# Performance work log

Measured on AMD Instinct MI355X. Metric: run time of the kernel, lower is better.

Reference implementation:

```python
import jax, jax.numpy as jnp
import numpy as np

B, C, L, D = 8, 32, 2048, 128
R, H = 8, 4  # num_routers, num_heads


def setup_inputs() -> dict:
    key = jax.random.key(0)
    ks = jax.random.split(key, 20)
    p = lambda k, shape: jax.random.normal(k, shape, dtype=jnp.float32) * 0.02
    inp = {
        "Z": jax.random.normal(ks[0], (B, C, L, D), dtype=jnp.float32),
        "router": p(ks[1], (R, D)),
        # router_sender projections (d_model -> d_model, torch Linear stored as x@W+b)
        "Wq1": p(ks[2], (D, D)), "bq1": jnp.zeros((D,), jnp.float32),
        "Wk1": p(ks[3], (D, D)), "bk1": jnp.zeros((D,), jnp.float32),
        "Wv1": p(ks[4], (D, D)), "bv1": jnp.zeros((D,), jnp.float32),
        "Wo1": p(ks[5], (D, D)), "bo1": jnp.zeros((D,), jnp.float32),
        # router_receiver projections
        "Wq2": p(ks[6], (D, D)), "bq2": jnp.zeros((D,), jnp.float32),
        "Wk2": p(ks[7], (D, D)), "bk2": jnp.zeros((D,), jnp.float32),
        "Wv2": p(ks[8], (D, D)), "bv2": jnp.zeros((D,), jnp.float32),
        "Wo2": p(ks[9], (D, D)), "bo2": jnp.zeros((D,), jnp.float32),
        # LayerNorm
        "gamma": jnp.ones((D,), jnp.float32),
        "beta": jnp.zeros((D,), jnp.float32),
    }
    return inp


def _cross_attn(q_in, k_in, v_in, Wq, bq, Wk, bk, Wv, bv, Wo, bo):
    # Informer FullAttention + AttentionLayer (dropout=0)
    Bn, Lq, Dm = q_in.shape
    Lk = k_in.shape[1]
    dh = Dm // H
    q = (q_in @ Wq + bq).reshape(Bn, Lq, H, dh)
    k = (k_in @ Wk + bk).reshape(Bn, Lk, H, dh)
    v = (v_in @ Wv + bv).reshape(Bn, Lk, H, dh)
    scale = 1.0 / np.sqrt(dh)
    scores = jnp.einsum("blhe,bshe->bhls", q, k) * scale
    A = jax.nn.softmax(scores, axis=-1)
    out = jnp.einsum("bhls,bshd->blhd", A, v).reshape(Bn, Lq, Dm)
    return out @ Wo + bo


def _layernorm(x, gamma, beta, eps=1e-5):
    mu = jnp.mean(x, axis=-1, keepdims=True)
    var = jnp.mean(jnp.square(x - mu), axis=-1, keepdims=True)
    return (x - mu) * jax.lax.rsqrt(var + eps) * gamma + beta


def reference(Z, router, Wq1, bq1, Wk1, bk1, Wv1, bv1, Wo1, bo1,
              Wq2, bq2, Wk2, bk2, Wv2, bv2, Wo2, bo2, gamma, beta):
    Bz, Cz, Lz, Dz = Z.shape
    x = Z.reshape(Bz * Cz, Lz, Dz)
    batch_router = jnp.broadcast_to(router[None], (Bz * Cz, R, Dz))
    # stage 1: routers attend to the sequence (R x L)
    router_buffer = _cross_attn(batch_router, x, x,
                                Wq1, bq1, Wk1, bk1, Wv1, bv1, Wo1, bo1)
    # stage 2: sequence attends to routers (L x R)
    router_receive = _cross_attn(x, router_buffer, router_buffer,
                                 Wq2, bq2, Wk2, bk2, Wv2, bv2, Wo2, bo2)
    out = _layernorm(x + router_receive, gamma, beta)
    return out.reshape(Bz, Cz, Lz, Dz)
```

## Files before the change

### kernel.cpp

```cpp
#include <hip/hip_runtime.h>

typedef float f4_t __attribute__((ext_vector_type(4)));
typedef __bf16 bf8_t __attribute__((ext_vector_type(8)));
typedef __bf16 bf4_t __attribute__((ext_vector_type(4)));

#define MFMA16(a,b,c) __builtin_amdgcn_mfma_f32_16x16x32_bf16((a),(b),(c),0,0,0)

static constexpr float kScale = 0.17677669529663687f;

__device__ __forceinline__ void bar_lds() {
  asm volatile("s_waitcnt lgkmcnt(0)" ::: "memory");
  __builtin_amdgcn_s_barrier();
}

__global__ __launch_bounds__(256) void k0_fold(
    const float* __restrict__ router, const float* __restrict__ Wq1,
    const float* __restrict__ bq1, const float* __restrict__ Wk1,
    const float* __restrict__ bk1, __bf16* __restrict__ q1t,
    float* __restrict__ c1)
{
  __shared__ float q1[8][132];
  const int t = threadIdx.x, b = blockIdx.x;
  {
    const int dp = t & 127, rh = t >> 7;
    float acc[4] = {0.f, 0.f, 0.f, 0.f};
#pragma unroll 4
    for (int e = 0; e < 128; ++e) {
      float wq = Wq1[e*128 + dp];
#pragma unroll
      for (int i = 0; i < 4; ++i)
        acc[i] += router[(rh*4 + i)*128 + e] * wq;
    }
#pragma unroll
    for (int i = 0; i < 4; ++i)
      q1[rh*4 + i][dp] = acc[i] + bq1[dp];
  }
  __syncthreads();
  {
    const int j = t & 31, h = j >> 3, r = j & 7;
    const int e = b*8 + (t >> 5);
    f4_t qv[8];
#pragma unroll
    for (int d4 = 0; d4 < 8; ++d4)
      qv[d4] = *(const f4_t*)&q1[r][h*32 + d4*4];
    float acc = 0.f;
#pragma unroll
    for (int d4 = 0; d4 < 8; ++d4) {
      f4_t wv = *(const f4_t*)(Wk1 + e*128 + h*32 + d4*4);
#pragma unroll
      for (int i = 0; i < 4; ++i) acc += qv[d4][i] * wv[i];
    }
    q1t[j*128 + e] = (__bf16)(acc * kScale);
  }
  if (b == 0 && t < 32) {
    int h = t >> 3, r = t & 7;
    float acc = 0.f;
    for (int d = 0; d < 32; ++d) acc += q1[r][h*32 + d] * bk1[h*32 + d];
    c1[t] = acc * kScale;
  }
}

__global__ __launch_bounds__(512) void k1_stage1(
    const float* __restrict__ Z, const __bf16* __restrict__ q1t_g,
    const float* __restrict__ c1_g, float* __restrict__ xap,
    float* __restrict__ lp, __bf16* __restrict__ xws)
{
  __shared__ __bf16 xb[64][136];
  __shared__ __bf16 xT[128][72];
  __shared__ __bf16 PT[32][72];
  __shared__ float lds_l[32];

  const int tid = threadIdx.x;
  const int bid = blockIdx.x;
  const float* xbase = Z + (size_t)bid * (256 * 128);
  __bf16* xwb = xws + (size_t)bid * (256 * 128);

  if (tid < 32) lds_l[tid] = 0.f;

  const int lane = tid & 63;
  const int w = tid >> 6;
  const int lc = lane & 15;
  const int lg = lane >> 4;
  const int ms = w >> 2;
  const int ns = w & 3;
  float c1v[4];
#pragma unroll
  for (int r2 = 0; r2 < 4; ++r2) c1v[r2] = c1_g[ms*16 + lg*4 + r2];
  bf8_t aq[4];
#pragma unroll
  for (int ks = 0; ks < 4; ++ks)
    aq[ks] = *(const bf8_t*)(q1t_g + (ms*16 + lc)*128 + ks*32 + lg*8);

  const f4_t fzero = {0.f, 0.f, 0.f, 0.f};
  f4_t accxa[2] = { fzero, fzero };
  float Lacc[4] = {0.f, 0.f, 0.f, 0.f};

  const int srow = tid >> 4;
  const int sd0  = (tid & 15) << 3;

  f4_t zr[4];
#pragma unroll
  for (int i = 0; i < 2; ++i) {
    const float* p = xbase + (srow + 32*i)*128 + sd0;
    zr[i*2]   = __builtin_nontemporal_load((const f4_t*)p);
    zr[i*2+1] = __builtin_nontemporal_load((const f4_t*)(p + 4));
  }

  bar_lds();

  for (int tile = 0; tile < 4; ++tile) {
#pragma unroll
    for (int i = 0; i < 2; ++i) {
      int pos = srow + 32*i;
      f4_t v0 = zr[i*2], v1 = zr[i*2+1];
      bf8_t b8 = { (__bf16)v0.x, (__bf16)v0.y, (__bf16)v0.z, (__bf16)v0.w,
                   (__bf16)v1.x, (__bf16)v1.y, (__bf16)v1.z, (__bf16)v1.w };
      *(bf8_t*)&xb[pos][sd0] = b8;
      *(bf8_t*)(xwb + (tile*64 + pos)*128 + sd0) = b8;
    }
    bar_lds();

    if (tile < 3) {
      const float* xt = xbase + (tile + 1) * (64 * 128);
#pragma unroll
      for (int i = 0; i < 2; ++i) {
        const float* p = xt + (srow + 32*i)*128 + sd0;
        zr[i*2]   = __builtin_nontemporal_load((const f4_t*)p);
        zr[i*2+1] = __builtin_nontemporal_load((const f4_t*)(p + 4));
      }
    }

#pragma unroll
    for (int s = 0; s < 2; ++s) {
      int u = tid + s*512;
      int dim = u & 127, pb = (u >> 7) << 3;
      bf8_t t8;
#pragma unroll
      for (int p = 0; p < 8; ++p) t8[p] = xb[pb + p][dim];
      *(bf8_t*)&xT[dim][pb] = t8;
    }
    f4_t sacc = fzero;
#pragma unroll
    for (int ks = 0; ks < 4; ++ks) {
      bf8_t b = *(const bf8_t*)&xb[ns*16 + lc][ks*32 + lg*8];
      sacc = MFMA16(aq[ks], b, sacc);
    }
    const int posn = ns*16 + lc;
#pragma unroll
    for (int r2 = 0; r2 < 4; ++r2) {
      float p = __expf(sacc[r2] + c1v[r2]);
      Lacc[r2] += p;
      PT[ms*16 + lg*4 + r2][posn] = (__bf16)p;
    }
    bar_lds();

#pragma unroll
    for (int nt = 0; nt < 2; ++nt) {
      const int dimt = (ns << 1) + nt;
#pragma unroll
      for (int ks = 0; ks < 2; ++ks) {
        bf8_t a = *(const bf8_t*)&xT[dimt*16 + lc][ks*32 + lg*8];
        bf8_t b = *(const bf8_t*)&PT[ms*16 + lc][ks*32 + lg*8];
        accxa[nt] = MFMA16(a, b, accxa[nt]);
      }
    }
  }

#pragma unroll
  for (int r2 = 0; r2 < 4; ++r2) {
    float v = Lacc[r2];
    v += __shfl_xor(v, 1);
    v += __shfl_xor(v, 2);
    v += __shfl_xor(v, 4);
    v += __shfl_xor(v, 8);
    if (lc == 0) atomicAdd(&lds_l[ms*16 + lg*4 + r2], v);
  }
  bar_lds();

  float* xo = xap + (size_t)bid * 4096;
  const int jrow = ms*16 + lc;
#pragma unroll
  for (int nt = 0; nt < 2; ++nt) {
    const int dim0 = ((ns << 1) + nt)*16 + lg*4;
    *(f4_t*)(xo + jrow*128 + dim0) = accxa[nt];
  }
  if (tid < 32) lp[bid*32 + tid] = lds_l[tid];
}

__global__ __launch_bounds__(256) void k1b_mid(
    const float* __restrict__ xap, const float* __restrict__ lp,
    const float* __restrict__ Wv1, const float* __restrict__ bv1,
    const float* __restrict__ Wo1, const float* __restrict__ bo1,
    const float* __restrict__ Wk2, const float* __restrict__ bk2,
    const float* __restrict__ Wv2, const float* __restrict__ bv2,
    const float* __restrict__ Wq2, const float* __restrict__ bq2,
    const float* __restrict__ Wo2,
    __bf16* __restrict__ kt2, float* __restrict__ c2, __bf16* __restrict__ vt2)
{
  __shared__ float xaT[128][33];
  __shared__ float invl[32];
  __shared__ float out1T[128][12];
  __shared__ float rbT[128][12];
  __shared__ float k2s[8][136];
  __shared__ float v2s[8][136];

  const int t = threadIdx.x, b = blockIdx.x;

  for (int idx = t; idx < 4096; idx += 256) {
    int j = idx >> 7, e = idx & 127;
    float s = 0.f;
#pragma unroll
    for (int k = 0; k < 8; ++k)
      s += xap[(size_t)(b*8 + k) * 4096 + idx];
    xaT[e][j] = s;
  }
  if (t < 32) {
    float s = 0.f;
#pragma unroll
    for (int k = 0; k < 8; ++k) s += lp[(b*8 + k)*32 + t];
    invl[t] = 1.f / s;
  }
  bar_lds();

  {
    const int hd = t & 127, rh = t >> 7, h = hd >> 5, j0 = h*8 + rh*4;
    float acc[4] = {0.f, 0.f, 0.f, 0.f};
#pragma unroll 4
    for (int e = 0; e < 128; ++e) {
      float wv = Wv1[e*128 + hd];
#pragma unroll
      for (int i = 0; i < 4; ++i) acc[i] += xaT[e][j0 + i] * wv;
    }
    float bv = bv1[hd];
#pragma unroll
    for (int i = 0; i < 4; ++i)
      out1T[hd][rh*4 + i] = acc[i] * invl[j0 + i] + bv;
  }
  bar_lds();

  {
    const int e2 = t & 127, rh = t >> 7;
    float acc[4] = {0.f, 0.f, 0.f, 0.f};
#pragma unroll 4
    for (int hd = 0; hd < 128; ++hd) {
      float wo = Wo1[hd*128 + e2];
#pragma unroll
      for (int i = 0; i < 4; ++i) acc[i] += out1T[hd][rh*4 + i] * wo;
    }
    float bo = bo1[e2];
#pragma unroll
    for (int i = 0; i < 4; ++i) rbT[e2][rh*4 + i] = acc[i] + bo;
  }
  bar_lds();

  {
    const int hd = t & 127, sel = t >> 7;
    const float* W  = sel ? Wv2 : Wk2;
    const float* bb = sel ? bv2 : bk2;
    float (*dst)[136] = sel ? v2s : k2s;
    float acc[8];
    float bbv = bb[hd];
#pragma unroll
    for (int r = 0; r < 8; ++r) acc[r] = bbv;
#pragma unroll 4
    for (int e = 0; e < 128; ++e) {
      float wv = W[e*128 + hd];
#pragma unroll
      for (int r = 0; r < 8; ++r) acc[r] += rbT[e][r] * wv;
    }
#pragma unroll
    for (int r = 0; r < 8; ++r) dst[r][hd] = acc[r];
  }
  bar_lds();

  {
    const int j = t & 31, h = j >> 3, r = j & 7;
    const int esub = t >> 5;
    f4_t k2v[8], v2v[8];
#pragma unroll
    for (int d4 = 0; d4 < 8; ++d4) {
      k2v[d4] = *(const f4_t*)&k2s[r][h*32 + d4*4];
      v2v[d4] = *(const f4_t*)&v2s[r][h*32 + d4*4];
    }
#pragma unroll
    for (int ei = 0; ei < 16; ++ei) {
      const int e = esub + ei*8;
      float acck = 0.f, accv = 0.f;
#pragma unroll
      for (int d4 = 0; d4 < 8; ++d4) {
        f4_t wq = *(const f4_t*)(Wq2 + e*128 + h*32 + d4*4);
#pragma unroll
        for (int i = 0; i < 4; ++i) {
          acck += wq[i] * k2v[d4][i];
          accv += v2v[d4][i] * Wo2[(h*32 + d4*4 + i)*128 + e];
        }
      }
      kt2[(size_t)b*4096 + j*128 + e] = (__bf16)(acck * kScale);
      vt2[(size_t)b*4096 + e*32 + j] = (__bf16)accv;
    }
  }
  if (t < 32) {
    int h = t >> 3, r = t & 7;
    float acc = 0.f;
#pragma unroll
    for (int d = 0; d < 32; ++d) acc += bq2[h*32 + d] * k2s[r][h*32 + d];
    c2[b*32 + t] = acc * kScale;
  }
}

__global__ __launch_bounds__(512) void k2_stage2(
    const __bf16* __restrict__ xws, const __bf16* __restrict__ kt2,
    const float* __restrict__ c2g, const __bf16* __restrict__ vt2,
    const float* __restrict__ bo2, const float* __restrict__ gamma,
    const float* __restrict__ beta, float* __restrict__ out)
{
  __shared__ __bf16 xb[128][136];
  __shared__ __bf16 P2[128][40];

  const int tid = threadIdx.x;
  const int blk = blockIdx.x;
  const int batch = blk >> 1;

  const __bf16* ktb = kt2 + (size_t)batch * 4096;
  const __bf16* vtb = vt2 + (size_t)batch * 4096;

  const int lane = tid & 63;
  const int w = tid >> 6;
  const int lc = lane & 15;
  const int lg = lane >> 4;

  float c2v[2] = { c2g[batch*32 + lc], c2g[batch*32 + 16 + lc] };
  f4_t bo2v[8], gv[8], bv[8];
#pragma unroll
  for (int nt = 0; nt < 8; ++nt) {
    int dd = nt*16 + lg*4;
    bo2v[nt] = *(const f4_t*)(bo2 + dd);
    gv[nt]   = *(const f4_t*)(gamma + dd);
    bv[nt]   = *(const f4_t*)(beta + dd);
  }
  bf8_t vfrag[8];
#pragma unroll
  for (int nt = 0; nt < 8; ++nt)
    vfrag[nt] = *(const bf8_t*)(vtb + (nt*16 + lc)*32 + lg*8);

  int spos[4], sd[4];
#pragma unroll
  for (int j = 0; j < 4; ++j) {
    int c = lane + j*64;
    spos[j] = w*16 + (c >> 4);
    sd[j]   = (c & 15) << 3;
  }

  const size_t base0 = (size_t)blk * 8 * 16384;
  uint4 zx[4];
#pragma unroll
  for (int j = 0; j < 4; ++j)
    zx[j] = *(const uint4*)(xws + base0 + spos[j]*128 + sd[j]);

  const f4_t fzero = {0.f, 0.f, 0.f, 0.f};

  for (int c = 0; c < 8; ++c) {
    const size_t cb = base0 + (size_t)c * 16384;
#pragma unroll
    for (int j = 0; j < 4; ++j)
      *(uint4*)&xb[spos[j]][sd[j]] = zx[j];
    if (c < 7) {
#pragma unroll
      for (int j = 0; j < 4; ++j)
        zx[j] = *(const uint4*)(xws + cb + 16384 + spos[j]*128 + sd[j]);
    }

    f4_t sacc[2] = { fzero, fzero };
#pragma unroll
    for (int ks = 0; ks < 4; ++ks) {
      bf8_t a = *(const bf8_t*)&xb[w*16 + lc][ks*32 + lg*8];
#pragma unroll
      for (int nt = 0; nt < 2; ++nt) {
        bf8_t b = *(const bf8_t*)(ktb + (nt*16 + lc)*128 + ks*32 + lg*8);
        sacc[nt] = MFMA16(a, b, sacc[nt]);
      }
    }
#pragma unroll
    for (int nt = 0; nt < 2; ++nt) {
#pragma unroll
      for (int r2 = 0; r2 < 4; ++r2) {
        float p = __expf(sacc[nt][r2] + c2v[nt]);
        float sum = p;
        sum += __shfl_xor(sum, 1);
        sum += __shfl_xor(sum, 2);
        sum += __shfl_xor(sum, 4);
        P2[w*16 + lg*4 + r2][nt*16 + lc] = (__bf16)(p * __builtin_amdgcn_rcpf(sum));
      }
    }

    bf8_t pf = *(const bf8_t*)&P2[w*16 + lc][lg*8];
    f4_t racc[8];
#pragma unroll
    for (int nt = 0; nt < 8; ++nt)
      racc[nt] = MFMA16(vfrag[nt], pf, fzero);

    const int pos = w*16 + lc;
    float s1 = 0.f, s2 = 0.f;
#pragma unroll
    for (int nt = 0; nt < 8; ++nt) {
      bf4_t xq = *(const bf4_t*)&xb[pos][nt*16 + lg*4];
#pragma unroll
      for (int r = 0; r < 4; ++r) {
        float tv = racc[nt][r] + bo2v[nt][r] + (float)xq[r];
        racc[nt][r] = tv;
        s1 += tv; s2 += tv*tv;
      }
    }
    s1 += __shfl_xor(s1, 16); s1 += __shfl_xor(s1, 32);
    s2 += __shfl_xor(s2, 16); s2 += __shfl_xor(s2, 32);
    float mean = s1 * (1.f/128.f);
    float var = s2 * (1.f/128.f) - mean*mean;
    float rstd = rsqrtf(var + 1e-5f);

    float* y = out + cb + (size_t)pos*128;
#pragma unroll
    for (int nt = 0; nt < 8; ++nt) {
      f4_t o;
#pragma unroll
      for (int r = 0; r < 4; ++r)
        o[r] = (racc[nt][r] - mean) * rstd * gv[nt][r] + bv[nt][r];
      __builtin_nontemporal_store(o, (f4_t*)(y + nt*16 + lg*4));
    }
  }
}

extern "C" void kernel_launch(void* const* d_in, const int* in_sizes, int n_in,
                              void* d_out, int out_size, void* d_ws, size_t ws_size,
                              hipStream_t stream)
{
  const float* Z     = (const float*)d_in[0];
  const float* router= (const float*)d_in[1];
  const float* Wq1   = (const float*)d_in[2];
  const float* bq1   = (const float*)d_in[3];
  const float* Wk1   = (const float*)d_in[4];
  const float* bk1   = (const float*)d_in[5];
  const float* Wv1   = (const float*)d_in[6];
  const float* bv1   = (const float*)d_in[7];
  const float* Wo1   = (const float*)d_in[8];
  const float* bo1   = (const float*)d_in[9];
  const float* Wq2   = (const float*)d_in[10];
  const float* bq2   = (const float*)d_in[11];
  const float* Wk2   = (const float*)d_in[12];
  const float* bk2   = (const float*)d_in[13];
  const float* Wv2   = (const float*)d_in[14];
  const float* bv2   = (const float*)d_in[15];
  const float* Wo2   = (const float*)d_in[16];
  const float* bo2   = (const float*)d_in[17];
  const float* gamma = (const float*)d_in[18];
  const float* beta  = (const float*)d_in[19];
  float* out = (float*)d_out;

  char* base = (char*)d_ws;
  __bf16* q1tb = (__bf16*)(base);
  float*  c1   = (float*)(base + 8192);
  float*  c2   = (float*)(base + 16384);
  float*  lp   = (float*)(base + 65536);
  float*  xap  = (float*)(base + (1u<<20));
  __bf16* kt2b = (__bf16*)(base + (36u<<20));
  __bf16* vt2b = (__bf16*)(base + (38u<<20));
  __bf16* xws  = (__bf16*)(base + (40u<<20));
  (void)in_sizes; (void)n_in; (void)out_size; (void)ws_size;

  k0_fold<<<dim3(16), dim3(256), 0, stream>>>(router, Wq1, bq1, Wk1, bk1, q1tb, c1);
  k1_stage1<<<dim3(2048), dim3(512), 0, stream>>>(Z, q1tb, c1, xap, lp, xws);
  k1b_mid<<<dim3(256), dim3(256), 0, stream>>>(xap, lp, Wv1, bv1, Wo1, bo1,
                                               Wk2, bk2, Wv2, bv2, Wq2, bq2, Wo2,
                                               kt2b, c2, vt2b);
  k2_stage2<<<dim3(512), dim3(512), 0, stream>>>(xws, kt2b, c2, vt2b, bo2, gamma, beta, out);
}
```

Before: 276.0 us.

## Fuse mid-stage router projections into stage-2 kernel, dropping a launch

```diff
diff --git a/kernel.cpp b/kernel.cpp
--- a/kernel.cpp
+++ b/kernel.cpp
@@ -187,95 +187,120 @@
   if (tid < 32) lp[bid*32 + tid] = lds_l[tid];
 }
 
-__global__ __launch_bounds__(256) void k1b_mid(
-    const float* __restrict__ xap, const float* __restrict__ lp,
+__global__ __launch_bounds__(512) void k2_stage2(
+    const __bf16* __restrict__ xws, const float* __restrict__ xap,
+    const float* __restrict__ lp,
     const float* __restrict__ Wv1, const float* __restrict__ bv1,
     const float* __restrict__ Wo1, const float* __restrict__ bo1,
     const float* __restrict__ Wk2, const float* __restrict__ bk2,
     const float* __restrict__ Wv2, const float* __restrict__ bv2,
     const float* __restrict__ Wq2, const float* __restrict__ bq2,
-    const float* __restrict__ Wo2,
-    __bf16* __restrict__ kt2, float* __restrict__ c2, __bf16* __restrict__ vt2)
+    const float* __restrict__ Wo2, const float* __restrict__ bo2,
+    const float* __restrict__ gamma, const float* __restrict__ beta,
+    float* __restrict__ out)
 {
-  __shared__ float xaT[128][33];
-  __shared__ float invl[32];
-  __shared__ float out1T[128][12];
-  __shared__ float rbT[128][12];
-  __shared__ float k2s[8][136];
-  __shared__ float v2s[8][136];
-
-  const int t = threadIdx.x, b = blockIdx.x;
-
-  for (int idx = t; idx < 4096; idx += 256) {
+  __shared__ __align__(16) char smem[64256];
+  __bf16 (*xb)[136]  = (__bf16 (*)[136])(smem);
+  __bf16 (*P2)[40]   = (__bf16 (*)[40])(smem + 34816);
+  __bf16 (*ktL)[136] = (__bf16 (*)[136])(smem + 45056);
+  __bf16 (*vtL)[40]  = (__bf16 (*)[40])(smem + 53760);
+  float* c2L  = (float*)(smem + 64000);
+  float* invl = (float*)(smem + 64128);
+  float (*xaT)[33]   = (float (*)[33])(smem);
+  float (*out1T)[12] = (float (*)[12])(smem + 16896);
+  float (*rbT)[12]   = (float (*)[12])(smem + 23040);
+  float (*k2s)[136]  = (float (*)[136])(smem);
+  float (*v2s)[136]  = (float (*)[136])(smem + 4352);
+
+  const int tid = threadIdx.x;
+  const int blk = blockIdx.x;
+  const int batch = blk >> 1;
+
+  const int lane = tid & 63;
+  const int w = tid >> 6;
+  const int lc = lane & 15;
+  const int lg = lane >> 4;
+
+  int spos[4], sd[4];
+#pragma unroll
+  for (int j = 0; j < 4; ++j) {
+    int c = lane + j*64;
+    spos[j] = w*16 + (c >> 4);
+    sd[j]   = (c & 15) << 3;
+  }
+  const size_t base0 = (size_t)blk * 8 * 16384;
+  uint4 zx[4];
+#pragma unroll
+  for (int j = 0; j < 4; ++j)
+    zx[j] = *(const uint4*)(xws + base0 + spos[j]*128 + sd[j]);
+
+#pragma unroll
+  for (int i = 0; i < 8; ++i) {
+    int idx = tid + i*512;
     int j = idx >> 7, e = idx & 127;
     float s = 0.f;
 #pragma unroll
     for (int k = 0; k < 8; ++k)
-      s += xap[(size_t)(b*8 + k) * 4096 + idx];
+      s += xap[(size_t)(batch*8 + k) * 4096 + idx];
     xaT[e][j] = s;
   }
-  if (t < 32) {
+  if (tid < 32) {
     float s = 0.f;
 #pragma unroll
-    for (int k = 0; k < 8; ++k) s += lp[(b*8 + k)*32 + t];
-    invl[t] = 1.f / s;
-  }
-  bar_lds();
-
-  {
-    const int hd = t & 127, rh = t >> 7, h = hd >> 5, j0 = h*8 + rh*4;
-    float acc[4] = {0.f, 0.f, 0.f, 0.f};
+    for (int k = 0; k < 8; ++k) s += lp[(batch*8 + k)*32 + tid];
+    invl[tid] = 1.f / s;
+  }
+  bar_lds();
+  {
+    const int hd = tid & 127, rh = tid >> 7, h = hd >> 5;
+    const int j0 = h*8 + rh*2;
+    float acc[2] = {0.f, 0.f};
 #pragma unroll 4
     for (int e = 0; e < 128; ++e) {
       float wv = Wv1[e*128 + hd];
-#pragma unroll
-      for (int i = 0; i < 4; ++i) acc[i] += xaT[e][j0 + i] * wv;
+      acc[0] += xaT[e][j0] * wv;
+      acc[1] += xaT[e][j0 + 1] * wv;
     }
     float bv = bv1[hd];
-#pragma unroll
-    for (int i = 0; i < 4; ++i)
-      out1T[hd][rh*4 + i] = acc[i] * invl[j0 + i] + bv;
-  }
-  bar_lds();
-
-  {
-    const int e2 = t & 127, rh = t >> 7;
-    float acc[4] = {0.f, 0.f, 0.f, 0.f};
+    out1T[hd][rh*2]     = acc[0] * invl[j0] + bv;
+    out1T[hd][rh*2 + 1] = acc[1] * invl[j0 + 1] + bv;
+  }
+  bar_lds();
+  {
+    const int e2 = tid & 127, rh = tid >> 7;
+    float acc[2] = {0.f, 0.f};
 #pragma unroll 4
     for (int hd = 0; hd < 128; ++hd) {
       float wo = Wo1[hd*128 + e2];
-#pragma unroll
-      for (int i = 0; i < 4; ++i) acc[i] += out1T[hd][rh*4 + i] * wo;
+      acc[0] += out1T[hd][rh*2] * wo;
+      acc[1] += out1T[hd][rh*2 + 1] * wo;
     }
     float bo = bo1[e2];
-#pragma unroll
-    for (int i = 0; i < 4; ++i) rbT[e2][rh*4 + i] = acc[i] + bo;
-  }
-  bar_lds();
-
-  {
-    const int hd = t & 127, sel = t >> 7;
+    rbT[e2][rh*2]     = acc[0] + bo;
+    rbT[e2][rh*2 + 1] = acc[1] + bo;
+  }
+  bar_lds();
+  {
+    const int hd = tid & 127, q = tid >> 7;
+    const int sel = q >> 1, r0 = (q & 1) * 4;
     const float* W  = sel ? Wv2 : Wk2;
     const float* bb = sel ? bv2 : bk2;
     float (*dst)[136] = sel ? v2s : k2s;
-    float acc[8];
     float bbv = bb[hd];
-#pragma unroll
-    for (int r = 0; r < 8; ++r) acc[r] = bbv;
+    float acc[4] = {bbv, bbv, bbv, bbv};
 #pragma unroll 4
     for (int e = 0; e < 128; ++e) {
       float wv = W[e*128 + hd];
 #pragma unroll
-      for (int r = 0; r < 8; ++r) acc[r] += rbT[e][r] * wv;
-    }
-#pragma unroll
-    for (int r = 0; r < 8; ++r) dst[r][hd] = acc[r];
-  }
-  bar_lds();
-
-  {
-    const int j = t & 31, h = j >> 3, r = j & 7;
-    const int esub = t >> 5;
+      for (int i = 0; i < 4; ++i) acc[i] += rbT[e][r0 + i] * wv;
+    }
+#pragma unroll
+    for (int i = 0; i < 4; ++i) dst[r0 + i][hd] = acc[i];
+  }
+  bar_lds();
+  {
+    const int j = tid & 31, h = j >> 3, r = j & 7;
+    const int esub = tid >> 5;
     f4_t k2v[8], v2v[8];
 #pragma unroll
     for (int d4 = 0; d4 < 8; ++d4) {
@@ -283,8 +308,8 @@
       v2v[d4] = *(const f4_t*)&v2s[r][h*32 + d4*4];
     }
 #pragma unroll
-    for (int ei = 0; ei < 16; ++ei) {
-      const int e = esub + ei*8;
+    for (int ei = 0; ei < 8; ++ei) {
+      const int e = esub + ei*16;
       float acck = 0.f, accv = 0.f;
 #pragma unroll
       for (int d4 = 0; d4 < 8; ++d4) {
@@ -295,41 +320,20 @@
           accv += v2v[d4][i] * Wo2[(h*32 + d4*4 + i)*128 + e];
         }
       }
-      kt2[(size_t)b*4096 + j*128 + e] = (__bf16)(acck * kScale);
-      vt2[(size_t)b*4096 + e*32 + j] = (__bf16)accv;
-    }
-  }
-  if (t < 32) {
-    int h = t >> 3, r = t & 7;
-    float acc = 0.f;
-#pragma unroll
-    for (int d = 0; d < 32; ++d) acc += bq2[h*32 + d] * k2s[r][h*32 + d];
-    c2[b*32 + t] = acc * kScale;
-  }
-}
-
-__global__ __launch_bounds__(512) void k2_stage2(
-    const __bf16* __restrict__ xws, const __bf16* __restrict__ kt2,
-    const float* __restrict__ c2g, const __bf16* __restrict__ vt2,
-    const float* __restrict__ bo2, const float* __restrict__ gamma,
-    const float* __restrict__ beta, float* __restrict__ out)
-{
-  __shared__ __bf16 xb[128][136];
-  __shared__ __bf16 P2[128][40];
-
-  const int tid = threadIdx.x;
-  const int blk = blockIdx.x;
-  const int batch = blk >> 1;
-
-  const __bf16* ktb = kt2 + (size_t)batch * 4096;
-  const __bf16* vtb = vt2 + (size_t)batch * 4096;
-
-  const int lane = tid & 63;
-  const int w = tid >> 6;
-  const int lc = lane & 15;
-  const int lg = lane >> 4;
-
-  float c2v[2] = { c2g[batch*32 + lc], c2g[batch*32 + 16 + lc] };
+      ktL[j][e] = (__bf16)(acck * kScale);
+      vtL[e][j] = (__bf16)accv;
+    }
+    if (tid < 32) {
+      int hh = tid >> 3, rr = tid & 7;
+      float acc = 0.f;
+#pragma unroll
+      for (int d = 0; d < 32; ++d) acc += bq2[hh*32 + d] * k2s[rr][hh*32 + d];
+      c2L[tid] = acc * kScale;
+    }
+  }
+  bar_lds();
+
+  float c2v[2] = { c2L[lc], c2L[16 + lc] };
   f4_t bo2v[8], gv[8], bv[8];
 #pragma unroll
   for (int nt = 0; nt < 8; ++nt) {
@@ -341,21 +345,7 @@
   bf8_t vfrag[8];
 #pragma unroll
   for (int nt = 0; nt < 8; ++nt)
-    vfrag[nt] = *(const bf8_t*)(vtb + (nt*16 + lc)*32 + lg*8);
-
-  int spos[4], sd[4];
-#pragma unroll
-  for (int j = 0; j < 4; ++j) {
-    int c = lane + j*64;
-    spos[j] = w*16 + (c >> 4);
-    sd[j]   = (c & 15) << 3;
-  }
-
-  const size_t base0 = (size_t)blk * 8 * 16384;
-  uint4 zx[4];
-#pragma unroll
-  for (int j = 0; j < 4; ++j)
-    zx[j] = *(const uint4*)(xws + base0 + spos[j]*128 + sd[j]);
+    vfrag[nt] = *(const bf8_t*)&vtL[nt*16 + lc][lg*8];
 
   const f4_t fzero = {0.f, 0.f, 0.f, 0.f};
 
@@ -376,7 +366,7 @@
       bf8_t a = *(const bf8_t*)&xb[w*16 + lc][ks*32 + lg*8];
 #pragma unroll
       for (int nt = 0; nt < 2; ++nt) {
-        bf8_t b = *(const bf8_t*)(ktb + (nt*16 + lc)*128 + ks*32 + lg*8);
+        bf8_t b = *(const bf8_t*)&ktL[nt*16 + lc][ks*32 + lg*8];
         sacc[nt] = MFMA16(a, b, sacc[nt]);
       }
     }
@@ -458,18 +448,16 @@
   char* base = (char*)d_ws;
   __bf16* q1tb = (__bf16*)(base);
   float*  c1   = (float*)(base + 8192);
-  float*  c2   = (float*)(base + 16384);
   float*  lp   = (float*)(base + 65536);
   float*  xap  = (float*)(base + (1u<<20));
-  __bf16* kt2b = (__bf16*)(base + (36u<<20));
-  __bf16* vt2b = (__bf16*)(base + (38u<<20));
   __bf16* xws  = (__bf16*)(base + (40u<<20));
   (void)in_sizes; (void)n_in; (void)out_size; (void)ws_size;
 
   k0_fold<<<dim3(16), dim3(256), 0, stream>>>(router, Wq1, bq1, Wk1, bk1, q1tb, c1);
   k1_stage1<<<dim3(2048), dim3(512), 0, stream>>>(Z, q1tb, c1, xap, lp, xws);
-  k1b_mid<<<dim3(256), dim3(256), 0, stream>>>(xap, lp, Wv1, bv1, Wo1, bo1,
-                                               Wk2, bk2, Wv2, bv2, Wq2, bq2, Wo2,
-                                               kt2b, c2, vt2b);
-  k2_stage2<<<dim3(512), dim3(512), 0, stream>>>(xws, kt2b, c2, vt2b, bo2, gamma, beta, out);
+  k2_stage2<<<dim3(512), dim3(512), 0, stream>>>(xws, xap, lp,
+                                                 Wv1, bv1, Wo1, bo1,
+                                                 Wk2, bk2, Wv2, bv2,
+                                                 Wq2, bq2, Wo2,
+                                                 bo2, gamma, beta, out);
 }
```

New measurement: 268.0 us. 1.03x faster.
